# Optimization experiments

Measured on AMD Instinct MI355X. Metric: run time of the kernel, lower is better.

The kernel has to match this reference:

```python
import jax, jax.numpy as jnp
import numpy as np

IN_SIZE = 1024
OUT_SIZE = 3 * IN_SIZE  # must equal 3*in_size for trigger_a * attn broadcast
B, S = 32, 512


def setup_inputs() -> dict:
    key = jax.random.key(0)
    ks = jax.random.split(key, 8)
    h_state = jax.random.normal(ks[0], (B, S, 2 * IN_SIZE), dtype=jnp.float32)
    x = jax.random.normal(ks[1], (B, S, IN_SIZE), dtype=jnp.float32)
    trigger = jax.random.randint(ks[2], (B,), 0, S)
    mask = jax.random.randint(ks[3], (B, S), 0, 2).astype(jnp.int32)
    # learned params (nn.Linear: y = x @ W.T + b; store pre-transposed as (in, out))
    Wa = jax.random.normal(ks[4], (3 * IN_SIZE, OUT_SIZE), dtype=jnp.float32) / np.sqrt(3 * IN_SIZE)
    ba = jnp.zeros((OUT_SIZE,), dtype=jnp.float32)
    Ws = jax.random.normal(ks[5], (2 * IN_SIZE, OUT_SIZE), dtype=jnp.float32) / np.sqrt(2 * IN_SIZE)
    bs = jnp.zeros((OUT_SIZE,), dtype=jnp.float32)
    return {"h_state": h_state, "x": x, "trigger": trigger, "mask": mask,
            "Wa": Wa, "ba": ba, "Ws": Ws, "bs": bs}


def reference(h_state, x, trigger, mask, Wa, ba, Ws, bs):
    # a: (B, S, 3*in_size)
    a = jnp.concatenate([h_state, x], axis=-1)
    b = a.shape[0]
    # one_hot + masked_select in the original == gather of the trigger row per batch
    trigger_a = a[jnp.arange(b), trigger]  # (B, 3*in_size)
    s = h_state.sum(axis=1)  # (B, 2*in_size)
    # et: (B, S, out_size)
    et = jnp.tanh(a @ Wa + ba + (s @ Ws + bs)[:, None, :])
    # masked_fill where mask == 0 (mask broadcast over feature dim)
    et = jnp.where(mask[:, :, None] == 0, jnp.float32(-1e9), et)
    # softmax over the FEATURE dim (dim=-1), as in the original; dropout in eval mode is identity
    attn = jax.nn.softmax(et, axis=-1)
    # trigger-weighted reduction over the sequence dim
    out = (trigger_a[:, None, :] * attn).sum(axis=1)  # (B, out_size)
    return out
```

## Files before the change

### kernel.cpp

```cpp
#include <hip/hip_runtime.h>
#include <hip/hip_bf16.h>
#include <hip/hip_fp16.h>


namespace {
constexpr int SIN  = 1024;
constexpr int KH   = 2048;
constexpr int NF   = 3072;
constexpr int NBAT = 32;
constexpr int NS   = 512;
constexpr int NM   = NBAT * NS;
constexpr int NDB  = NF / 64;
constexpr int KC   = 8;
constexpr int NKT  = NF / 64;
constexpr int NCH  = 8;
}

typedef unsigned short u16;
typedef __bf16 bf16x8 __attribute__((ext_vector_type(8)));
typedef float  f32x4  __attribute__((ext_vector_type(4)));

#define ASYNC_CP16(gptr, lptr)                                                              \
  __builtin_amdgcn_global_load_lds((__attribute__((address_space(1))) void*)(gptr),         \
                                   (__attribute__((address_space(3))) void*)(lptr), 16, 0, 0)

__device__ __forceinline__ u16 f2b(float f) {
  union { float f; unsigned u; } v; v.f = f;
  unsigned u = v.u;
  u += 0x7FFFu + ((u >> 16) & 1u);
  return (u16)(u >> 16);
}

__device__ __forceinline__ unsigned pk2(float a, float b) {
  return (unsigned)f2b(a) | ((unsigned)f2b(b) << 16);
}

__global__ __launch_bounds__(256) void k_prep(const int* __restrict__ mask,
                                              int* __restrict__ bcnt,
                                              int* __restrict__ boff,
                                              int* __restrict__ meta) {
  int tid = threadIdx.x;
  int b = tid >> 3, seg = tid & 7;
  int c = 0;
#pragma unroll
  for (int i = 0; i < 64; ++i) c += mask[b * NS + seg * 64 + i];
  c += __shfl_xor(c, 1, 64);
  c += __shfl_xor(c, 2, 64);
  c += __shfl_xor(c, 4, 64);
  __shared__ int sc[NBAT];
  if (seg == 0) { sc[b] = c; bcnt[b] = c; }
  __syncthreads();
  if (tid == 0) {
    int run = 0;
    for (int bb = 0; bb < NBAT; ++bb) { boff[bb] = run; run += sc[bb]; }
    meta[0] = run;
    meta[1] = (run + 255) & ~255;
  }
}

__global__ __launch_bounds__(512) void k_gather(const int* __restrict__ mask,
                                                const int* __restrict__ boff,
                                                const int* __restrict__ meta,
                                                int* __restrict__ rowmap) {
  __shared__ int ps[NS];
  int b = blockIdx.x, t = threadIdx.x;
  int m = mask[b * NS + t];
  ps[t] = m;
  __syncthreads();
#pragma unroll
  for (int off = 1; off < NS; off <<= 1) {
    int v = (t >= off) ? ps[t - off] : 0;
    __syncthreads();
    ps[t] += v;
    __syncthreads();
  }
  if (m) rowmap[boff[b] + ps[t] - m] = b * NS + t;
  if (b == 0) {
    int Mc = meta[0], McPad = meta[1];
    if (Mc + t < McPad) rowmap[Mc + t] = 0;
  }
}

__global__ __launch_bounds__(256) void k_sum_h(const float* __restrict__ h,
                                               float* __restrict__ s) {
  int b = blockIdx.x;
  int d = blockIdx.y * 256 + threadIdx.x;
  const float* p = h + (size_t)b * NS * KH + d;
  float acc = 0.f;
#pragma unroll 8
  for (int t = 0; t < NS; ++t) acc += p[(size_t)t * KH];
  s[b * KH + d] = acc;
}

__global__ __launch_bounds__(256) void k_base1(const float* __restrict__ s,
                                               const float* __restrict__ Ws,
                                               float* __restrict__ basep) {
  __shared__ float sT[NBAT][KH / KC];
  int f  = blockIdx.x * 256 + threadIdx.x;
  int k0 = blockIdx.y * (KH / KC);
  for (int it = 0; it < NBAT; ++it) {
    int idx = it * 256 + threadIdx.x;
    int b = idx >> 8, kk = idx & 255;
    sT[b][kk] = s[b * KH + k0 + kk];
  }
  __syncthreads();
  float acc[NBAT] = {};
  for (int k = 0; k < KH / KC; k += 4) {
    float w0 = Ws[(size_t)(k0 + k + 0) * NF + f];
    float w1 = Ws[(size_t)(k0 + k + 1) * NF + f];
    float w2 = Ws[(size_t)(k0 + k + 2) * NF + f];
    float w3 = Ws[(size_t)(k0 + k + 3) * NF + f];
#pragma unroll
    for (int b = 0; b < NBAT; ++b) {
      float4 sv = *(const float4*)&sT[b][k];
      acc[b] += sv.x * w0 + sv.y * w1 + sv.z * w2 + sv.w * w3;
    }
  }
#pragma unroll
  for (int b = 0; b < NBAT; ++b)
    basep[((size_t)blockIdx.y * NBAT + b) * NF + f] = acc[b];
}

__global__ __launch_bounds__(256) void k_base2(const float* __restrict__ basep,
                                               const float* __restrict__ ba,
                                               const float* __restrict__ bs,
                                               float* __restrict__ base) {
  int b = blockIdx.x;
  int f = blockIdx.y * 256 + threadIdx.x;
  float acc = 0.f;
#pragma unroll
  for (int kc = 0; kc < KC; ++kc) acc += basep[((size_t)kc * NBAT + b) * NF + f];
  base[b * NF + f] = acc + ba[f] + bs[f];
}

__global__ __launch_bounds__(256) void k_cvt_a(const float* __restrict__ h,
                                               const float* __restrict__ x,
                                               const int* __restrict__ rowmap,
                                               const int* __restrict__ meta,
                                               u16* __restrict__ A) {
  const int total = meta[1] * (NF / 8);
  for (int idx = blockIdx.x * 256 + threadIdx.x; idx < total;
       idx += gridDim.x * 256) {
    int i = idx / (NF / 8);
    int k = (idx - i * (NF / 8)) * 8;
    uint4 o;
    if (i >= meta[0]) {
      o.x = o.y = o.z = o.w = 0u;
    } else {
      int ro = rowmap[i];
      int b = ro >> 9, t = ro & 511;
      const float* src = (k < KH) ? h + ((size_t)b * NS + t) * KH + k
                                  : x + ((size_t)b * NS + t) * SIN + (k - KH);
      float4 v0 = *(const float4*)src;
      float4 v1 = *(const float4*)(src + 4);
      o.x = pk2(v0.x, v0.y); o.y = pk2(v0.z, v0.w);
      o.z = pk2(v1.x, v1.y); o.w = pk2(v1.z, v1.w);
    }
    *(uint4*)(A + (size_t)i * NF + k) = o;
  }
}

__global__ __launch_bounds__(256) void k_wat(const float* __restrict__ Wa,
                                             u16* __restrict__ WaT) {
  __shared__ float tile[64][65];
  int k0 = blockIdx.x * 64, f0 = blockIdx.y * 64;
  int tid = threadIdx.x;
  int col4 = (tid & 15) * 4, row = tid >> 4;
#pragma unroll
  for (int rr = 0; rr < 64; rr += 16) {
    float4 v = *(const float4*)(Wa + (size_t)(k0 + row + rr) * NF + f0 + col4);
    tile[row + rr][col4 + 0] = v.x; tile[row + rr][col4 + 1] = v.y;
    tile[row + rr][col4 + 2] = v.z; tile[row + rr][col4 + 3] = v.w;
  }
  __syncthreads();
#pragma unroll
  for (int rr = 0; rr < 64; rr += 16) {
    int f = f0 + row + rr;
    ushort4 o;
    o.x = f2b(tile[col4 + 0][row + rr]); o.y = f2b(tile[col4 + 1][row + rr]);
    o.z = f2b(tile[col4 + 2][row + rr]); o.w = f2b(tile[col4 + 3][row + rr]);
    *(ushort4*)(WaT + (size_t)f * NF + k0 + col4) = o;
  }
}

#define LDSOFF(row, gg) ((row) * 32 + ((((gg) ^ (((row) >> 1) & 3))) << 3))

#define LDB4(BUF, KS)                                                        \
  _Pragma("unroll") for (int nf = 0; nf < 4; ++nf) {                         \
    int rb = wc * 64 + nf * 16 + lr;                                         \
    bfr[nf] = *(const bf16x8*)&lds[BUF][1][KS][LDSOFF(rb, g)];               \
  }

#define LDA4(BUF, KS, MH)                                                    \
  _Pragma("unroll") for (int mf = 0; mf < 4; ++mf) {                         \
    int ra = wr * 128 + ((MH) * 4 + mf) * 16 + lr;                           \
    afr[mf] = *(const bf16x8*)&lds[BUF][0][KS][LDSOFF(ra, g)];               \
  }

#define MFMA16(MH)                                                           \
  _Pragma("unroll") for (int mf = 0; mf < 4; ++mf)                           \
  _Pragma("unroll") for (int nf = 0; nf < 4; ++nf)                           \
    acc[(MH) * 4 + mf][nf] = __builtin_amdgcn_mfma_f32_16x16x32_bf16(        \
        afr[mf], bfr[nf], acc[(MH) * 4 + mf][nf], 0, 0, 0);

#define STAGE(SMAT, SBUF, SKS, SKT)                                          \
  if ((SKT) < NKT) {                                                         \
    _Pragma("unroll") for (int q = 0; q < 2; ++q) {                          \
      const u16* src = ((SMAT) ? pB[q] : pA[q]) + (SKT) * 64 + (SKS) * 32;   \
      ASYNC_CP16(src, &lds[SBUF][SMAT][SKS][q * 4096 + wid * 512]);          \
    }                                                                        \
  }

#define PH(BUF, KS, MH, SMAT, SBUF, SKS, SKT, BAR)                           \
  {                                                                          \
    if ((MH) == 0) { LDB4(BUF, KS) }                                         \
    LDA4(BUF, KS, MH)                                                        \
    STAGE(SMAT, SBUF, SKS, SKT)                                              \
    __builtin_amdgcn_s_setprio(1);                                           \
    MFMA16(MH)                                                               \
    __builtin_amdgcn_s_setprio(0);                                           \
    if ((BAR) == 2) asm volatile("s_waitcnt vmcnt(4)" ::: "memory");         \
    if (BAR) __builtin_amdgcn_s_barrier();                                   \
  }

__global__ __launch_bounds__(512, 2) void k_gemm(const u16* __restrict__ A,
                                                 const u16* __restrict__ Wt,
                                                 const float* __restrict__ base,
                                                 const int* __restrict__ rowmap,
                                                 const int* __restrict__ meta,
                                                 __half* __restrict__ P,
                                                 float* __restrict__ Dpart) {
  __shared__ __align__(16) u16 lds[2][2][2][8192];
  const int MT   = meta[1] >> 8;
  const int nact = MT * 12;
  const int flat = blockIdx.x;
  if (flat >= nact) return;
  const int qx = nact >> 3, rx = nact & 7;
  const int xcd = flat & 7, idx = flat >> 3;
  const int swz = (xcd < rx) ? xcd * (qx + 1) + idx
                             : rx * (qx + 1) + (xcd - rx) * qx + idx;
  const int mt = swz / 12, nt = swz - mt * 12;
  const int r0 = mt << 8, c0 = nt << 8;

  const int tid = threadIdx.x;
  const int wid = tid >> 6, lane = tid & 63;
  const int wr = wid >> 2, wc = wid & 3;
  const int g = lane >> 4, lr = lane & 15;

  const u16* pA[2]; const u16* pB[2];
#pragma unroll
  for (int q = 0; q < 2; ++q) {
    int c = q * 512 + tid;
    int row = c >> 2;
    int kc8 = (((c & 3) ^ ((row >> 1) & 3)) << 3);
    pA[q] = A  + (size_t)(r0 + row) * NF + kc8;
    pB[q] = Wt + (size_t)(c0 + row) * NF + kc8;
  }

  f32x4 acc[8][4] = {};
  bf16x8 afr[4], bfr[4];

  STAGE(0, 0, 0, 0) STAGE(1, 0, 0, 0)
  STAGE(0, 0, 1, 0) STAGE(1, 0, 1, 0)
  STAGE(0, 1, 0, 1) STAGE(1, 1, 0, 1)
  asm volatile("s_waitcnt vmcnt(4)" ::: "memory");
  __builtin_amdgcn_s_barrier();

#pragma unroll 1
  for (int i = 0; i < NKT / 2; ++i) {
    const int kt1 = 2 * i + 1, kt2 = 2 * i + 2, kt3 = 2 * i + 3;
    PH(0, 0, 0, 0, 1, 1, kt1, 0)
    PH(0, 0, 1, 1, 1, 1, kt1, 1)
    PH(0, 1, 0, 0, 0, 0, kt2, 0)
    PH(0, 1, 1, 1, 0, 0, kt2, 2)
    PH(1, 0, 0, 0, 0, 1, kt2, 0)
    PH(1, 0, 1, 1, 0, 1, kt2, 1)
    PH(1, 1, 0, 0, 1, 0, kt3, 0)
    PH(1, 1, 1, 1, 1, 0, kt3, 2)
  }

  const int cbase = c0 + wc * 64;
#pragma unroll
  for (int mf = 0; mf < 8; ++mf) {
#pragma unroll
    for (int j = 0; j < 4; ++j) {
      int i = r0 + wr * 128 + mf * 16 + g * 4 + j;
      int b = rowmap[i] >> 9;
      float rs = 0.f;
#pragma unroll
      for (int nf = 0; nf < 4; ++nf) {
        int ccn = cbase + nf * 16 + lr;
        float z  = acc[mf][nf][j] + base[b * NF + ccn];
        z        = fminf(fmaxf(z, -15.f), 15.f);
        float e2 = __expf(2.f * z);
        float th = (e2 - 1.f) / (e2 + 1.f);
        float p  = __expf(th);
        P[(size_t)i * NF + ccn] = __float2half(p);
        rs += p;
      }
#pragma unroll
      for (int off = 1; off < 16; off <<= 1) rs += __shfl_xor(rs, off, 64);
      if (lr == 0) Dpart[(size_t)i * NDB + (cbase >> 6)] = rs;
    }
  }
}

__global__ __launch_bounds__(256) void k_final1(const __half* __restrict__ P,
                                                const float* __restrict__ Dpart,
                                                const int* __restrict__ boff,
                                                const int* __restrict__ bcnt,
                                                float* __restrict__ pb) {
  int c = blockIdx.x;
  int b = c >> 3, j = c & 7;
  int f = blockIdx.y * 1024 + threadIdx.x * 4;
  int cnt = bcnt[b];
  int lo = j * 64, hi = min(cnt, lo + 64);
  int off = boff[b];
  __shared__ float ivs[64];
  if (threadIdx.x < 64) {
    int t = lo + threadIdx.x;
    if (t < hi) {
      const float* dp = Dpart + (size_t)(off + t) * NDB;
      float d = 0.f;
#pragma unroll
      for (int q = 0; q < NDB; ++q) d += dp[q];
      ivs[threadIdx.x] = 1.0f / d;
    }
  }
  __syncthreads();
  float a0 = 0.f, a1 = 0.f, a2 = 0.f, a3 = 0.f;
  for (int t = lo; t < hi; ++t) {
    const __half2* hp = (const __half2*)(P + (size_t)(off + t) * NF + f);
    __half2 h0 = hp[0], h1 = hp[1];
    float2 f0 = __half22float2(h0), f1 = __half22float2(h1);
    float iv = ivs[t - lo];
    a0 += f0.x * iv; a1 += f0.y * iv; a2 += f1.x * iv; a3 += f1.y * iv;
  }
  float4 o; o.x = a0; o.y = a1; o.z = a2; o.w = a3;
  *(float4*)(pb + (size_t)c * NF + f) = o;
}

__global__ __launch_bounds__(256) void k_final2(const float* __restrict__ pb,
                                                const int* __restrict__ bcnt,
                                                const float* __restrict__ h,
                                                const float* __restrict__ x,
                                                const int* __restrict__ trig,
                                                float* __restrict__ out) {
  int b = blockIdx.x;
  int f = blockIdx.y * 256 + threadIdx.x;
  float acc = 0.f;
#pragma unroll
  for (int j = 0; j < NCH; ++j) acc += pb[(size_t)(b * NCH + j) * NF + f];
  acc += (float)(NS - bcnt[b]) * (1.0f / (float)NF);
  int tr = trig[b];
  float ta = (f < KH) ? h[((size_t)b * NS + tr) * KH + f]
                      : x[((size_t)b * NS + tr) * SIN + f - KH];
  out[b * NF + f] = acc * ta;
}

extern "C" void kernel_launch(void* const* d_in, const int* in_sizes, int n_in,
                              void* d_out, int out_size, void* d_ws, size_t ws_size,
                              hipStream_t stream) {
  const float* h_state = (const float*)d_in[0];
  const float* x       = (const float*)d_in[1];
  const int*   trigger = (const int*)d_in[2];
  const int*   mask    = (const int*)d_in[3];
  const float* Wa      = (const float*)d_in[4];
  const float* ba      = (const float*)d_in[5];
  const float* Ws      = (const float*)d_in[6];
  const float* bs      = (const float*)d_in[7];
  float*       out     = (float*)d_out;

  char* w = (char*)d_ws;
  u16*    Abf   = (u16*)w;                 w += (size_t)NM * NF * 2;
  u16*    WaT   = (u16*)w;                 w += (size_t)NF * NF * 2;
  __half* P     = (__half*)w;              w += (size_t)NM * NF * 2;
  float*  s     = (float*)w;               w += (size_t)NBAT * KH * 4;
  float*  base  = (float*)w;               w += (size_t)NBAT * NF * 4;
  float*  Dpart = (float*)w;               w += (size_t)NM * NDB * 4;
  float*  basep = (float*)Dpart;
  float*  pb    = (float*)w;               w += (size_t)NBAT * NCH * NF * 4;
  int*    rowmap= (int*)w;                 w += (size_t)NM * 4;
  int*    bcnt  = (int*)w;                 w += 128;
  int*    boff  = (int*)w;                 w += 128;
  int*    meta  = (int*)w;                 w += 128;

  (void)in_sizes; (void)n_in; (void)out_size; (void)ws_size;

  k_prep  <<<dim3(1), 256, 0, stream>>>(mask, bcnt, boff, meta);
  k_gather<<<dim3(NBAT), 512, 0, stream>>>(mask, boff, meta, rowmap);
  k_sum_h <<<dim3(NBAT, KH / 256), 256, 0, stream>>>(h_state, s);
  k_cvt_a <<<dim3(2048), 256, 0, stream>>>(h_state, x, rowmap, meta, Abf);
  k_wat   <<<dim3(NF / 64, NF / 64), 256, 0, stream>>>(Wa, WaT);
  k_base1 <<<dim3(NF / 256, KC), 256, 0, stream>>>(s, Ws, basep);
  k_base2 <<<dim3(NBAT, NF / 256), 256, 0, stream>>>(basep, ba, bs, base);
  k_gemm  <<<dim3((NF / 256) * (NM / 256)), 512, 0, stream>>>(Abf, WaT, base, rowmap, meta, P, Dpart);
  k_final1<<<dim3(NBAT * NCH, NF / 1024), 256, 0, stream>>>(P, Dpart, boff, bcnt, pb);
  k_final2<<<dim3(NBAT, NF / 256), 256, 0, stream>>>(pb, bcnt, h_state, x, trigger, out);
}
```

Measured before the change: 389.6 us.

## Fuse h_state column sum with bf16 gather-conversion of masked rows

Merges the separate h_state sum kernel and the gather-convert kernel into one pass that reads h_state and x once, accumulating per-chunk partial sums while scattering masked rows as bf16 into the compacted A matrix by a precomputed rank. The gather kernel now also writes a rank array and zeroes the padding rows, and base1 reduces the partial sums itself. This removes a second full read of h_state (about 128MB) at the cost of scattered 2-byte stores instead of vectorized 16-byte stores.

```diff
diff --git a/kernel.cpp b/kernel.cpp
--- a/kernel.cpp
+++ b/kernel.cpp
@@ -61,7 +61,9 @@
 __global__ __launch_bounds__(512) void k_gather(const int* __restrict__ mask,
                                                 const int* __restrict__ boff,
                                                 const int* __restrict__ meta,
-                                                int* __restrict__ rowmap) {
+                                                int* __restrict__ rowmap,
+                                                int* __restrict__ rank,
+                                                u16* __restrict__ A) {
   __shared__ int ps[NS];
   int b = blockIdx.x, t = threadIdx.x;
   int m = mask[b * NS + t];
@@ -74,25 +76,68 @@
     ps[t] += v;
     __syncthreads();
   }
-  if (m) rowmap[boff[b] + ps[t] - m] = b * NS + t;
-  if (b == 0) {
-    int Mc = meta[0], McPad = meta[1];
-    if (Mc + t < McPad) rowmap[Mc + t] = 0;
-  }
-}
-
-__global__ __launch_bounds__(256) void k_sum_h(const float* __restrict__ h,
-                                               float* __restrict__ s) {
-  int b = blockIdx.x;
-  int d = blockIdx.y * 256 + threadIdx.x;
-  const float* p = h + (size_t)b * NS * KH + d;
-  float acc = 0.f;
-#pragma unroll 8
-  for (int t = 0; t < NS; ++t) acc += p[(size_t)t * KH];
-  s[b * KH + d] = acc;
-}
-
-__global__ __launch_bounds__(256) void k_base1(const float* __restrict__ s,
+  if (m) {
+    int idx = boff[b] + ps[t] - 1;
+    rowmap[idx] = b * NS + t;
+    rank[b * NS + t] = idx;
+  }
+  int Mc = meta[0], pad = meta[1] - Mc;
+  if (b == 0 && t < 256) { if (t < pad) rowmap[Mc + t] = 0; }
+  for (int r = b; r < pad; r += NBAT) {
+    unsigned* row = (unsigned*)(A + (size_t)(Mc + r) * NF);
+    for (int u = t; u < NF / 2; u += 512) row[u] = 0;
+  }
+}
+
+__global__ __launch_bounds__(256) void k_sumcvt(const float* __restrict__ h,
+                                                const float* __restrict__ x,
+                                                const int* __restrict__ mask,
+                                                const int* __restrict__ rank,
+                                                float* __restrict__ spart,
+                                                u16* __restrict__ A) {
+  int c = blockIdx.x;
+  int b = c >> 3, tc = c & 7;
+  int cb = blockIdx.y, tid = threadIdx.x;
+  __shared__ int ms[64];
+  __shared__ int rk[64];
+  if (tid < 64) {
+    int t = tc * 64 + tid;
+    int m = mask[b * NS + t];
+    ms[tid] = m;
+    rk[tid] = m ? rank[b * NS + t] : 0;
+  }
+  __syncthreads();
+  if (cb < 8) {
+    int d = cb * 256 + tid;
+    const float* hb = h + ((size_t)b * NS + tc * 64) * KH + d;
+    float acc = 0.f;
+    for (int t0 = 0; t0 < 64; t0 += 8) {
+      float v[8];
+#pragma unroll
+      for (int u = 0; u < 8; ++u) v[u] = hb[(size_t)(t0 + u) * KH];
+#pragma unroll
+      for (int u = 0; u < 8; ++u) {
+        acc += v[u];
+        if (ms[t0 + u]) A[(size_t)rk[t0 + u] * NF + d] = f2b(v[u]);
+      }
+    }
+    spart[(size_t)c * KH + d] = acc;
+  } else {
+    int d = (cb - 8) * 256 + tid;
+    const float* xb = x + ((size_t)b * NS + tc * 64) * SIN + d;
+    for (int t0 = 0; t0 < 64; t0 += 8) {
+      float v[8];
+#pragma unroll
+      for (int u = 0; u < 8; ++u) v[u] = xb[(size_t)(t0 + u) * SIN];
+#pragma unroll
+      for (int u = 0; u < 8; ++u) {
+        if (ms[t0 + u]) A[(size_t)rk[t0 + u] * NF + KH + d] = f2b(v[u]);
+      }
+    }
+  }
+}
+
+__global__ __launch_bounds__(256) void k_base1(const float* __restrict__ spart,
                                                const float* __restrict__ Ws,
                                                float* __restrict__ basep) {
   __shared__ float sT[NBAT][KH / KC];
@@ -100,8 +145,12 @@
   int k0 = blockIdx.y * (KH / KC);
   for (int it = 0; it < NBAT; ++it) {
     int idx = it * 256 + threadIdx.x;
-    int b = idx >> 8, kk = idx & 255;
-    sT[b][kk] = s[b * KH + k0 + kk];
+    int bb = idx >> 8, kk = idx & 255;
+    float v = 0.f;
+#pragma unroll
+    for (int tc = 0; tc < NCH; ++tc)
+      v += spart[(size_t)(bb * NCH + tc) * KH + k0 + kk];
+    sT[bb][kk] = v;
   }
   __syncthreads();
   float acc[NBAT] = {};
@@ -131,33 +180,6 @@
 #pragma unroll
   for (int kc = 0; kc < KC; ++kc) acc += basep[((size_t)kc * NBAT + b) * NF + f];
   base[b * NF + f] = acc + ba[f] + bs[f];
-}
-
-__global__ __launch_bounds__(256) void k_cvt_a(const float* __restrict__ h,
-                                               const float* __restrict__ x,
-                                               const int* __restrict__ rowmap,
-                                               const int* __restrict__ meta,
-                                               u16* __restrict__ A) {
-  const int total = meta[1] * (NF / 8);
-  for (int idx = blockIdx.x * 256 + threadIdx.x; idx < total;
-       idx += gridDim.x * 256) {
-    int i = idx / (NF / 8);
-    int k = (idx - i * (NF / 8)) * 8;
-    uint4 o;
-    if (i >= meta[0]) {
-      o.x = o.y = o.z = o.w = 0u;
-    } else {
-      int ro = rowmap[i];
-      int b = ro >> 9, t = ro & 511;
-      const float* src = (k < KH) ? h + ((size_t)b * NS + t) * KH + k
-                                  : x + ((size_t)b * NS + t) * SIN + (k - KH);
-      float4 v0 = *(const float4*)src;
-      float4 v1 = *(const float4*)(src + 4);
-      o.x = pk2(v0.x, v0.y); o.y = pk2(v0.z, v0.w);
-      o.z = pk2(v1.x, v1.y); o.w = pk2(v1.z, v1.w);
-    }
-    *(uint4*)(A + (size_t)i * NF + k) = o;
-  }
 }
 
 __global__ __launch_bounds__(256) void k_wat(const float* __restrict__ Wa,
@@ -375,12 +397,13 @@
   u16*    Abf   = (u16*)w;                 w += (size_t)NM * NF * 2;
   u16*    WaT   = (u16*)w;                 w += (size_t)NF * NF * 2;
   __half* P     = (__half*)w;              w += (size_t)NM * NF * 2;
-  float*  s     = (float*)w;               w += (size_t)NBAT * KH * 4;
+  float*  spart = (float*)w;               w += (size_t)NBAT * NCH * KH * 4;
   float*  base  = (float*)w;               w += (size_t)NBAT * NF * 4;
   float*  Dpart = (float*)w;               w += (size_t)NM * NDB * 4;
   float*  basep = (float*)Dpart;
   float*  pb    = (float*)w;               w += (size_t)NBAT * NCH * NF * 4;
   int*    rowmap= (int*)w;                 w += (size_t)NM * 4;
+  int*    rank  = (int*)w;                 w += (size_t)NM * 4;
   int*    bcnt  = (int*)w;                 w += 128;
   int*    boff  = (int*)w;                 w += 128;
   int*    meta  = (int*)w;                 w += 128;
@@ -388,11 +411,10 @@
   (void)in_sizes; (void)n_in; (void)out_size; (void)ws_size;
 
   k_prep  <<<dim3(1), 256, 0, stream>>>(mask, bcnt, boff, meta);
-  k_gather<<<dim3(NBAT), 512, 0, stream>>>(mask, boff, meta, rowmap);
-  k_sum_h <<<dim3(NBAT, KH / 256), 256, 0, stream>>>(h_state, s);
-  k_cvt_a <<<dim3(2048), 256, 0, stream>>>(h_state, x, rowmap, meta, Abf);
+  k_gather<<<dim3(NBAT), 512, 0, stream>>>(mask, boff, meta, rowmap, rank, Abf);
+  k_sumcvt<<<dim3(NBAT * NCH, 12), 256, 0, stream>>>(h_state, x, mask, rank, spart, Abf);
   k_wat   <<<dim3(NF / 64, NF / 64), 256, 0, stream>>>(Wa, WaT);
-  k_base1 <<<dim3(NF / 256, KC), 256, 0, stream>>>(s, Ws, basep);
+  k_base1 <<<dim3(NF / 256, KC), 256, 0, stream>>>(spart, Ws, basep);
   k_base2 <<<dim3(NBAT, NF / 256), 256, 0, stream>>>(basep, ba, bs, base);
   k_gemm  <<<dim3((NF / 256) * (NM / 256)), 512, 0, stream>>>(Abf, WaT, base, rowmap, meta, P, Dpart);
   k_final1<<<dim3(NBAT * NCH, NF / 1024), 256, 0, stream>>>(P, Dpart, boff, bcnt, pb);
```

Result: slower. 437.5 us (+12.3%).
